# Optimization experiments

Hardware: AMD Instinct MI355X
Metric: run time of the kernel (lower is better)

Reference implementation:

```python
import jax, jax.numpy as jnp
import numpy as np

N, S, D, DOUT, ATTEN, NUM_ATTR = 10000, 20, 512, 512, 64, 9

def setup_inputs() -> dict:
    key = jax.random.key(0)
    ks = jax.random.split(key, 9)
    return {
        "self_vecs": jax.random.normal(ks[0], (N, D), dtype=jnp.float32),
        "neigh_vecs": jax.random.normal(ks[1], (N, S, D), dtype=jnp.float32),
        "neigh_weight": jax.random.uniform(ks[2], (N, S, 1), dtype=jnp.float32),
        "neigh_column": jax.random.randint(ks[3], (N, S, 1), 0, NUM_ATTR, dtype=jnp.int32),
        "neigh_weights": jax.random.normal(ks[4], (D, DOUT), dtype=jnp.float32) * (1.0 / np.sqrt(D)),
        "self_weights": jax.random.normal(ks[5], (D, DOUT), dtype=jnp.float32) * (1.0 / np.sqrt(D)),
        "alpha": jax.random.normal(ks[6], (NUM_ATTR,), dtype=jnp.float32),
        "self_atten": jax.random.normal(ks[7], (D, ATTEN), dtype=jnp.float32) * (1.0 / np.sqrt(D)),
        "neigh_atten": jax.random.normal(ks[8], (D, ATTEN), dtype=jnp.float32) * (1.0 / np.sqrt(D)),
        "v": jax.random.normal(jax.random.fold_in(key, 99), (ATTEN, 1), dtype=jnp.float32) * (1.0 / np.sqrt(ATTEN)),
    }

def reference(self_vecs, neigh_vecs, neigh_weight, neigh_column,
              neigh_weights, self_weights, alpha, self_atten, neigh_atten, v):
    # per-neighbor edge weighting
    nv = neigh_vecs * neigh_weight                      # [N,S,D]
    # gather alpha by attribute column, softmax over neighbors (axis=1)
    a = alpha[neigh_column[..., 0]][..., None]          # [N,S,1]
    a_exp = jnp.exp(a)
    atten = a_exp / jnp.sum(a_exp, axis=1, keepdims=True)
    nv = nv * atten
    # dropout = 0.0 -> identity
    neigh_sum = jnp.sum(nv, axis=1)                     # [N,D]
    from_neighs = neigh_sum @ neigh_weights             # [N,DOUT]
    from_self = self_vecs @ self_weights                # [N,DOUT]
    self_ai = self_vecs @ self_atten                    # [N,ATTEN]
    neigh_ai = neigh_sum @ neigh_atten                  # [N,ATTEN]
    imp_self = self_ai + self_ai
    imp_neigh = neigh_ai + self_ai
    a_self = jnp.exp(jnp.tanh(imp_self @ v))            # [N,1]
    a_neigh = jnp.exp(jnp.tanh(imp_neigh @ v))          # [N,1]
    denom = a_self + a_neigh
    out = (a_self / denom) * from_self + (a_neigh / denom) * from_neighs
    return jax.nn.relu(out)
```

## Files before the change

### kernel.cpp

```cpp
#include <hip/hip_runtime.h>
#include <hip/hip_bf16.h>

#define N_NODES 10000
#define S_NB 20
#define D_IN 512
#define D_OUT 512
#define ATTEN_D 64
#define KTOT 1024
#define M_PAD 10048

typedef __bf16 bf16_t;
typedef bf16_t bf16x8 __attribute__((ext_vector_type(8)));
typedef float f32x4 __attribute__((ext_vector_type(4)));

__device__ __forceinline__ unsigned short f2bf(float f) {
    unsigned int u = __float_as_uint(f);
    unsigned int r = u + 0x7FFFu + ((u >> 16) & 1u);
    return (unsigned short)(r >> 16);
}

__device__ __forceinline__ void gl_lds16(const unsigned short* g, unsigned short* l) {
    __builtin_amdgcn_global_load_lds(
        (const __attribute__((address_space(1))) void*)g,
        (__attribute__((address_space(3))) void*)l,
        16, 0, 0);
}

__global__ void prep_kernel(const float* __restrict__ neigh_w,
                            const float* __restrict__ self_w,
                            const float* __restrict__ self_atten,
                            const float* __restrict__ neigh_atten,
                            const float* __restrict__ v,
                            float* __restrict__ u_self, float* __restrict__ u_neigh,
                            unsigned short* __restrict__ Wt,
                            unsigned short* __restrict__ X) {
    int idx = blockIdx.x * blockDim.x + threadIdx.x;
    int stride = gridDim.x * blockDim.x;

    for (int i = idx; i < D_OUT * KTOT; i += stride) {
        int n = i >> 10;
        int k = i & (KTOT - 1);
        float w = (k < D_IN) ? self_w[k * D_OUT + n] : neigh_w[(k - D_IN) * D_OUT + n];
        Wt[i] = f2bf(w);
    }
    for (int i = idx; i < 2 * D_IN; i += stride) {
        const float* row = (i < D_IN) ? (self_atten + (size_t)i * ATTEN_D)
                                      : (neigh_atten + (size_t)(i - D_IN) * ATTEN_D);
        float s = 0.f;
        #pragma unroll
        for (int j = 0; j < ATTEN_D; ++j) s = fmaf(row[j], v[j], s);
        if (i < D_IN) u_self[i] = s; else u_neigh[i - D_IN] = s;
    }
    for (int i = idx; i < (M_PAD - N_NODES) * KTOT; i += stride) {
        X[(size_t)N_NODES * KTOT + i] = 0;
    }
}

__global__ __launch_bounds__(128) void aggregate_kernel(
        const float* __restrict__ self_vecs, const float* __restrict__ neigh_vecs,
        const float* __restrict__ neigh_weight, const int* __restrict__ neigh_column,
        const float* __restrict__ alpha,
        const float* __restrict__ u_self, const float* __restrict__ u_neigh,
        unsigned short* __restrict__ X) {
    const int n = blockIdx.x;
    const int tid = threadIdx.x;

    __shared__ float coef[S_NB];
    __shared__ float red[4];
    __shared__ float gates[2];

    if (tid < 64) {
        float e = 0.f, wgt = 0.f;
        if (tid < S_NB) {
            e = expf(alpha[neigh_column[n * S_NB + tid]]);
            wgt = neigh_weight[n * S_NB + tid];
        }
        float s = e;
        #pragma unroll
        for (int off = 32; off > 0; off >>= 1) s += __shfl_down(s, off, 64);
        s = __shfl(s, 0, 64);
        if (tid < S_NB) coef[tid] = wgt * e / s;
    }
    __syncthreads();

    const float4* nb = (const float4*)(neigh_vecs + (size_t)n * S_NB * D_IN);
    float4 acc = make_float4(0.f, 0.f, 0.f, 0.f);
    #pragma unroll
    for (int s = 0; s < S_NB; ++s) {
        float4 t = nb[s * 128 + tid];
        float c = coef[s];
        acc.x = fmaf(c, t.x, acc.x);
        acc.y = fmaf(c, t.y, acc.y);
        acc.z = fmaf(c, t.z, acc.z);
        acc.w = fmaf(c, t.w, acc.w);
    }
    float4 sv = ((const float4*)(self_vecs + (size_t)n * D_IN))[tid];
    float4 us = ((const float4*)u_self)[tid];
    float4 un = ((const float4*)u_neigh)[tid];
    float p1 = sv.x * us.x + sv.y * us.y + sv.z * us.z + sv.w * us.w;
    float p2 = acc.x * un.x + acc.y * un.y + acc.z * un.z + acc.w * un.w;

    #pragma unroll
    for (int off = 32; off > 0; off >>= 1) {
        p1 += __shfl_down(p1, off, 64);
        p2 += __shfl_down(p2, off, 64);
    }
    int lane = tid & 63, wid = tid >> 6;
    if (lane == 0) { red[wid * 2] = p1; red[wid * 2 + 1] = p2; }
    __syncthreads();
    if (tid == 0) {
        float s1 = red[0] + red[2];
        float s2 = red[1] + red[3];
        float a_s = expf(tanhf(2.0f * s1));
        float a_n = expf(tanhf(s2 + s1));
        float inv = 1.0f / (a_s + a_n);
        gates[0] = a_s * inv;
        gates[1] = a_n * inv;
    }
    __syncthreads();
    float gs = gates[0], gn = gates[1];

    unsigned short* xrow = X + (size_t)n * KTOT;
    ushort4 o;
    o.x = f2bf(gs * sv.x); o.y = f2bf(gs * sv.y);
    o.z = f2bf(gs * sv.z); o.w = f2bf(gs * sv.w);
    *(ushort4*)(xrow + tid * 4) = o;
    o.x = f2bf(gn * acc.x); o.y = f2bf(gn * acc.y);
    o.z = f2bf(gn * acc.z); o.w = f2bf(gn * acc.w);
    *(ushort4*)(xrow + D_IN + tid * 4) = o;
}

#define BM 64
#define BN 128
#define BK 64

__global__ __launch_bounds__(256) void gemm_kernel(
        const unsigned short* __restrict__ X, const unsigned short* __restrict__ Wt,
        float* __restrict__ out) {
    __shared__ __align__(16) unsigned short As[BM * BK];
    __shared__ __align__(16) unsigned short Bs[BN * BK];
    const int tid = threadIdx.x;
    const int lane = tid & 63;
    const int wid = tid >> 6;
    const int m0 = blockIdx.y * BM;
    const int n0 = blockIdx.x * BN;
    const int wm = (wid >> 1) * 32;
    const int wn = (wid & 1) * 64;
    const int quad = lane >> 4;
    const int mrow = lane & 15;

    f32x4 acc[2][4];
    f32x4 zero = {0.f, 0.f, 0.f, 0.f};
    #pragma unroll
    for (int i = 0; i < 2; ++i)
        #pragma unroll
        for (int j = 0; j < 4; ++j) acc[i][j] = zero;

    const int srow = tid >> 3;
    const int skp  = (tid & 7) * 8;
    const unsigned short* gA0 = X  + (size_t)(m0 + srow) * KTOT + skp;
    const unsigned short* gA1 = X  + (size_t)(m0 + 32 + srow) * KTOT + skp;
    const unsigned short* gB0 = Wt + (size_t)(n0 + srow) * KTOT + skp;
    const unsigned short* gB1 = Wt + (size_t)(n0 + 32 + srow) * KTOT + skp;
    const unsigned short* gB2 = Wt + (size_t)(n0 + 64 + srow) * KTOT + skp;
    const unsigned short* gB3 = Wt + (size_t)(n0 + 96 + srow) * KTOT + skp;
    unsigned short* lA0 = As + tid * 8;
    unsigned short* lA1 = As + 2048 + tid * 8;
    unsigned short* lB0 = Bs + tid * 8;
    unsigned short* lB1 = Bs + 2048 + tid * 8;
    unsigned short* lB2 = Bs + 4096 + tid * 8;
    unsigned short* lB3 = Bs + 6144 + tid * 8;

    for (int k0 = 0; k0 < KTOT; k0 += BK) {
        __syncthreads();
        gl_lds16(gA0 + k0, lA0);
        gl_lds16(gA1 + k0, lA1);
        gl_lds16(gB0 + k0, lB0);
        gl_lds16(gB1 + k0, lB1);
        gl_lds16(gB2 + k0, lB2);
        gl_lds16(gB3 + k0, lB3);
        __syncthreads();

        #pragma unroll
        for (int s = 0; s < 2; ++s) {
            bf16x8 a[2], b[4];
            #pragma unroll
            for (int i = 0; i < 2; ++i)
                a[i] = *(const bf16x8*)(As + (wm + i * 16 + mrow) * BK + s * 32 + quad * 8);
            #pragma unroll
            for (int j = 0; j < 4; ++j)
                b[j] = *(const bf16x8*)(Bs + (wn + j * 16 + mrow) * BK + s * 32 + quad * 8);
            #pragma unroll
            for (int i = 0; i < 2; ++i)
                #pragma unroll
                for (int j = 0; j < 4; ++j)
                    acc[i][j] = __builtin_amdgcn_mfma_f32_16x16x32_bf16(a[i], b[j], acc[i][j], 0, 0, 0);
        }
    }

    #pragma unroll
    for (int i = 0; i < 2; ++i) {
        int rbase = m0 + wm + i * 16 + quad * 4;
        #pragma unroll
        for (int j = 0; j < 4; ++j) {
            int c = n0 + wn + j * 16 + mrow;
            #pragma unroll
            for (int r = 0; r < 4; ++r) {
                int R = rbase + r;
                if (R < N_NODES)
                    out[(size_t)R * D_OUT + c] = fmaxf(acc[i][j][r], 0.f);
            }
        }
    }
}

extern "C" void kernel_launch(void* const* d_in, const int* in_sizes, int n_in,
                              void* d_out, int out_size, void* d_ws, size_t ws_size,
                              hipStream_t stream) {
    const float* self_vecs     = (const float*)d_in[0];
    const float* neigh_vecs    = (const float*)d_in[1];
    const float* neigh_weight  = (const float*)d_in[2];
    const int*   neigh_column  = (const int*)d_in[3];
    const float* neigh_weights = (const float*)d_in[4];
    const float* self_weights  = (const float*)d_in[5];
    const float* alpha         = (const float*)d_in[6];
    const float* self_atten    = (const float*)d_in[7];
    const float* neigh_atten   = (const float*)d_in[8];
    const float* v             = (const float*)d_in[9];
    float* out = (float*)d_out;

    char* ws = (char*)d_ws;
    float* u_self  = (float*)ws;
    float* u_neigh = u_self + D_IN;
    unsigned short* Wt = (unsigned short*)(ws + 4096);
    unsigned short* X  = (unsigned short*)(ws + 4096 + (size_t)D_OUT * KTOT * 2);

    hipLaunchKernelGGL(prep_kernel, dim3(1024), dim3(256), 0, stream,
                       neigh_weights, self_weights, self_atten, neigh_atten, v,
                       u_self, u_neigh, Wt, X);
    hipLaunchKernelGGL(aggregate_kernel, dim3(N_NODES), dim3(128), 0, stream,
                       self_vecs, neigh_vecs, neigh_weight, neigh_column, alpha,
                       u_self, u_neigh, X);
    hipLaunchKernelGGL(gemm_kernel, dim3(D_OUT / BN, M_PAD / BM), dim3(256), 0, stream,
                       X, Wt, out);
}
```

Baseline: 595.5 us.

## Map one wavefront per node in aggregation, removing LDS and block barriers

```diff
diff --git a/kernel.cpp b/kernel.cpp
--- a/kernel.cpp
+++ b/kernel.cpp
@@ -12,6 +12,7 @@
 typedef __bf16 bf16_t;
 typedef bf16_t bf16x8 __attribute__((ext_vector_type(8)));
 typedef float f32x4 __attribute__((ext_vector_type(4)));
+typedef unsigned short u16x8 __attribute__((ext_vector_type(8)));
 
 __device__ __forceinline__ unsigned short f2bf(float f) {
     unsigned int u = __float_as_uint(f);
@@ -56,78 +57,71 @@
     }
 }
 
-__global__ __launch_bounds__(128) void aggregate_kernel(
+__global__ __launch_bounds__(256) void aggregate_kernel(
         const float* __restrict__ self_vecs, const float* __restrict__ neigh_vecs,
         const float* __restrict__ neigh_weight, const int* __restrict__ neigh_column,
         const float* __restrict__ alpha,
         const float* __restrict__ u_self, const float* __restrict__ u_neigh,
         unsigned short* __restrict__ X) {
-    const int n = blockIdx.x;
-    const int tid = threadIdx.x;
-
-    __shared__ float coef[S_NB];
-    __shared__ float red[4];
-    __shared__ float gates[2];
-
-    if (tid < 64) {
-        float e = 0.f, wgt = 0.f;
-        if (tid < S_NB) {
-            e = expf(alpha[neigh_column[n * S_NB + tid]]);
-            wgt = neigh_weight[n * S_NB + tid];
-        }
-        float s = e;
-        #pragma unroll
-        for (int off = 32; off > 0; off >>= 1) s += __shfl_down(s, off, 64);
-        s = __shfl(s, 0, 64);
-        if (tid < S_NB) coef[tid] = wgt * e / s;
-    }
-    __syncthreads();
+    const int lane = threadIdx.x & 63;
+    const int n = blockIdx.x * 4 + (threadIdx.x >> 6);
+
+    float e = 0.f, wgt = 0.f;
+    if (lane < S_NB) {
+        e = expf(alpha[neigh_column[n * S_NB + lane]]);
+        wgt = neigh_weight[n * S_NB + lane];
+    }
+    float ssum = e;
+    #pragma unroll
+    for (int off = 32; off > 0; off >>= 1) ssum += __shfl_xor(ssum, off, 64);
+    float coefv = wgt * e / ssum;
 
     const float4* nb = (const float4*)(neigh_vecs + (size_t)n * S_NB * D_IN);
-    float4 acc = make_float4(0.f, 0.f, 0.f, 0.f);
+    float4 acc0 = make_float4(0.f, 0.f, 0.f, 0.f);
+    float4 acc1 = make_float4(0.f, 0.f, 0.f, 0.f);
     #pragma unroll
     for (int s = 0; s < S_NB; ++s) {
-        float4 t = nb[s * 128 + tid];
-        float c = coef[s];
-        acc.x = fmaf(c, t.x, acc.x);
-        acc.y = fmaf(c, t.y, acc.y);
-        acc.z = fmaf(c, t.z, acc.z);
-        acc.w = fmaf(c, t.w, acc.w);
-    }
-    float4 sv = ((const float4*)(self_vecs + (size_t)n * D_IN))[tid];
-    float4 us = ((const float4*)u_self)[tid];
-    float4 un = ((const float4*)u_neigh)[tid];
-    float p1 = sv.x * us.x + sv.y * us.y + sv.z * us.z + sv.w * us.w;
-    float p2 = acc.x * un.x + acc.y * un.y + acc.z * un.z + acc.w * un.w;
-
+        float c = __shfl(coefv, s, 64);
+        float4 x0 = nb[s * 128 + 2 * lane];
+        float4 x1 = nb[s * 128 + 2 * lane + 1];
+        acc0.x = fmaf(c, x0.x, acc0.x); acc0.y = fmaf(c, x0.y, acc0.y);
+        acc0.z = fmaf(c, x0.z, acc0.z); acc0.w = fmaf(c, x0.w, acc0.w);
+        acc1.x = fmaf(c, x1.x, acc1.x); acc1.y = fmaf(c, x1.y, acc1.y);
+        acc1.z = fmaf(c, x1.z, acc1.z); acc1.w = fmaf(c, x1.w, acc1.w);
+    }
+
+    const float4* svp = (const float4*)(self_vecs + (size_t)n * D_IN);
+    float4 sv0 = svp[2 * lane], sv1 = svp[2 * lane + 1];
+    float4 us0 = ((const float4*)u_self)[2 * lane];
+    float4 us1 = ((const float4*)u_self)[2 * lane + 1];
+    float4 un0 = ((const float4*)u_neigh)[2 * lane];
+    float4 un1 = ((const float4*)u_neigh)[2 * lane + 1];
+    float p1 = sv0.x * us0.x + sv0.y * us0.y + sv0.z * us0.z + sv0.w * us0.w
+             + sv1.x * us1.x + sv1.y * us1.y + sv1.z * us1.z + sv1.w * us1.w;
+    float p2 = acc0.x * un0.x + acc0.y * un0.y + acc0.z * un0.z + acc0.w * un0.w
+             + acc1.x * un1.x + acc1.y * un1.y + acc1.z * un1.z + acc1.w * un1.w;
     #pragma unroll
     for (int off = 32; off > 0; off >>= 1) {
-        p1 += __shfl_down(p1, off, 64);
-        p2 += __shfl_down(p2, off, 64);
-    }
-    int lane = tid & 63, wid = tid >> 6;
-    if (lane == 0) { red[wid * 2] = p1; red[wid * 2 + 1] = p2; }
-    __syncthreads();
-    if (tid == 0) {
-        float s1 = red[0] + red[2];
-        float s2 = red[1] + red[3];
-        float a_s = expf(tanhf(2.0f * s1));
-        float a_n = expf(tanhf(s2 + s1));
-        float inv = 1.0f / (a_s + a_n);
-        gates[0] = a_s * inv;
-        gates[1] = a_n * inv;
-    }
-    __syncthreads();
-    float gs = gates[0], gn = gates[1];
+        p1 += __shfl_xor(p1, off, 64);
+        p2 += __shfl_xor(p2, off, 64);
+    }
+    float a_s = expf(tanhf(2.0f * p1));
+    float a_n = expf(tanhf(p2 + p1));
+    float inv = 1.0f / (a_s + a_n);
+    float gs = a_s * inv, gn = a_n * inv;
 
     unsigned short* xrow = X + (size_t)n * KTOT;
-    ushort4 o;
-    o.x = f2bf(gs * sv.x); o.y = f2bf(gs * sv.y);
-    o.z = f2bf(gs * sv.z); o.w = f2bf(gs * sv.w);
-    *(ushort4*)(xrow + tid * 4) = o;
-    o.x = f2bf(gn * acc.x); o.y = f2bf(gn * acc.y);
-    o.z = f2bf(gn * acc.z); o.w = f2bf(gn * acc.w);
-    *(ushort4*)(xrow + D_IN + tid * 4) = o;
+    u16x8 o;
+    o[0] = f2bf(gs * sv0.x); o[1] = f2bf(gs * sv0.y);
+    o[2] = f2bf(gs * sv0.z); o[3] = f2bf(gs * sv0.w);
+    o[4] = f2bf(gs * sv1.x); o[5] = f2bf(gs * sv1.y);
+    o[6] = f2bf(gs * sv1.z); o[7] = f2bf(gs * sv1.w);
+    *(u16x8*)(xrow + 8 * lane) = o;
+    o[0] = f2bf(gn * acc0.x); o[1] = f2bf(gn * acc0.y);
+    o[2] = f2bf(gn * acc0.z); o[3] = f2bf(gn * acc0.w);
+    o[4] = f2bf(gn * acc1.x); o[5] = f2bf(gn * acc1.y);
+    o[6] = f2bf(gn * acc1.z); o[7] = f2bf(gn * acc1.w);
+    *(u16x8*)(xrow + D_IN + 8 * lane) = o;
 }
 
 #define BM 64
@@ -238,7 +232,7 @@
     hipLaunchKernelGGL(prep_kernel, dim3(1024), dim3(256), 0, stream,
                        neigh_weights, self_weights, self_atten, neigh_atten, v,
                        u_self, u_neigh, Wt, X);
-    hipLaunchKernelGGL(aggregate_kernel, dim3(N_NODES), dim3(128), 0, stream,
+    hipLaunchKernelGGL(aggregate_kernel, dim3(N_NODES / 4), dim3(256), 0, stream,
                        self_vecs, neigh_vecs, neigh_weight, neigh_column, alpha,
                        u_self, u_neigh, X);
     hipLaunchKernelGGL(gemm_kernel, dim3(D_OUT / BN, M_PAD / BM), dim3(256), 0, stream,
```

After: 594.2 us. About the same (-0.2%).
